# Kernel tuning notes

Measured on AMD Instinct MI355X. Metric: run time of the kernel, lower is better.

## Reference

```python
import jax, jax.numpy as jnp
import numpy as np

C = 256
EPS = 1e-5


def setup_inputs() -> dict:
    key = jax.random.key(0)
    ks = jax.random.split(key, 10)
    B, H, W = 4, 64, 64
    x1 = jax.random.normal(ks[0], (B, C, H, W), dtype=jnp.float32)
    x2 = jax.random.normal(ks[1], (B, C, H, W), dtype=jnp.float32)
    s = 1.0 / np.sqrt(C)
    qw = jax.random.normal(ks[2], (C, C), dtype=jnp.float32) * s
    qb = jax.random.normal(ks[3], (C,), dtype=jnp.float32) * 0.01
    kw = jax.random.normal(ks[4], (C, C), dtype=jnp.float32) * s
    kb = jax.random.normal(ks[5], (C,), dtype=jnp.float32) * 0.01
    vw = jax.random.normal(ks[6], (C, C), dtype=jnp.float32) * s
    vb = jax.random.normal(ks[7], (C,), dtype=jnp.float32) * 0.01
    ln_w = jnp.ones((C,), dtype=jnp.float32)
    ln_b = jnp.zeros((C,), dtype=jnp.float32)
    return {"x1": x1, "x2": x2, "qw": qw, "qb": qb, "kw": kw, "kb": kb,
            "vw": vw, "vb": vb, "ln_w": ln_w, "ln_b": ln_b}


def _conv1x1(x, w, b):
    # 1x1 conv == per-pixel matmul over channels. x: [B,C,H,W], w: [O,C]
    return jnp.einsum('oc,bchw->bohw', w, x) + b[None, :, None, None]


def reference(x1, x2, qw, qb, kw, kb, vw, vb, ln_w, ln_b):
    q = _conv1x1(x1, qw, qb)   # [B,C,H,W]
    k = _conv1x1(x2, kw, kb)   # [B,C,H,W]
    v = _conv1x1(x2, vw, vb)   # [B,C,H,W]
    # scores: [B,H,W,I,J]; softmax over LAST axis (j) only, as in the torch code
    scores = jnp.einsum('bchw,bcij->bhwij', q, k)
    attn = jax.nn.softmax(scores, axis=-1)
    fusion = jnp.einsum('bhwij,bcij->bchw', attn, v)  # [B,C,H,W]
    # LayerNorm2d: normalize over channel dim per spatial location
    mean = jnp.mean(fusion, axis=1, keepdims=True)
    var = jnp.var(fusion, axis=1, keepdims=True)
    normed = (fusion - mean) * jax.lax.rsqrt(var + EPS)
    return normed * ln_w[None, :, None, None] + ln_b[None, :, None, None]
```

## Files before the change

kernel.cpp:

```cpp
#include <hip/hip_runtime.h>


#define CDIM 256
#define NPOS 4096
#define BATCH 4
#define EPSV 1e-5f

typedef _Float16 f16;
typedef __attribute__((ext_vector_type(8))) _Float16 f16x8;
typedef __attribute__((ext_vector_type(4))) float f32x4;
typedef __attribute__((ext_vector_type(16))) float f32x16;

#define WST       264
#define QK_STRIDE 264
#define S_STRIDE  68
#define DQ_STRIDE 72
#define F_STRIDE  68

#define LBAR() asm volatile("s_waitcnt lgkmcnt(0)\n\ts_barrier" ::: "memory")


static __device__ __forceinline__ f16x8 cvt8(const float* __restrict__ p) {
    float4 w0 = *(const float4*)p;
    float4 w1 = *(const float4*)(p + 4);
    f16x8 r;
    r[0] = (f16)w0.x; r[1] = (f16)w0.y; r[2] = (f16)w0.z; r[3] = (f16)w0.w;
    r[4] = (f16)w1.x; r[5] = (f16)w1.y; r[6] = (f16)w1.z; r[7] = (f16)w1.w;
    return r;
}

__global__ __launch_bounds__(256, 4) void prep_kernel(
    const float* __restrict__ x1, const float* __restrict__ x2,
    const float* __restrict__ qw, const float* __restrict__ kw,
    const float* __restrict__ vw,
    f16* __restrict__ X1T, f16* __restrict__ X2T, f16* __restrict__ W16)
{
    const int id = blockIdx.x;
    const int t  = threadIdx.x;
    if (id < 2048) {
        __shared__ f16 T[64 * 72];
        const float* xs = (id & 1) ? x2 : x1;
        f16* dst        = (id & 1) ? X2T : X1T;
        const int t2 = id >> 1;
        const int b  = t2 >> 8;
        const int rm = t2 & 255;
        const int c0 = (rm >> 6) * 64;
        const int n0 = (rm & 63) * 64;
        const float* src = xs + ((size_t)b * CDIM + c0) * NPOS + n0;
        const int rr = t >> 6, col = t & 63;
        #pragma unroll
        for (int j = 0; j < 16; ++j) {
            int row = rr + j * 4;
            T[col * 72 + row] = (f16)src[(size_t)row * NPOS + col];
        }
        __syncthreads();
        const int n = t >> 3, lc = (t & 7) * 8;
        f16* d0 = dst + ((size_t)b * NPOS + n0) * CDIM + c0;
        #pragma unroll
        for (int j = 0; j < 2; ++j) {
            int nn = n + j * 32;
            *(f16x8*)(d0 + (size_t)nn * CDIM + lc) = *(const f16x8*)&T[nn * 72 + lc];
        }
    } else {
        const int wblk = id - 2048;
        const int pr = wblk >> 2, h = wblk & 3;
        const float* W = (pr == 0 ? qw : pr == 1 ? kw : vw) + (size_t)h * 64 * CDIM;
        f16* D = W16 + (size_t)pr * CDIM * CDIM + (size_t)h * 64 * CDIM;
        #pragma unroll
        for (int i = 0; i < 8; ++i) {
            int g = t + i * 256;
            int row = g >> 5, col = (g & 31) * 8;
            *(f16x8*)(D + (size_t)row * CDIM + col) = cvt8(W + (size_t)row * CDIM + col);
        }
    }
}

__global__ __launch_bounds__(256, 2) void gemm_kernel(
    const f16* __restrict__ X1T, const f16* __restrict__ X2T,
    const f16* __restrict__ W16,
    const float* __restrict__ qb, const float* __restrict__ kb,
    const float* __restrict__ vb,
    f16* __restrict__ Qg, f16* __restrict__ Kg, f16* __restrict__ Vg)
{
    __shared__ f16 Xs[64 * WST];
    __shared__ f16 Wh[64 * WST];
    __shared__ f16 Ds[64 * DQ_STRIDE];
    __shared__ float biasS[256];

    const int id = blockIdx.x;
    const int pr  = id >> 8;
    const int rem = id & 255;
    const int b   = rem >> 6;
    const int p0  = (rem & 63) << 6;
    const f16* XT = (pr == 0) ? X1T : X2T;
    const f16* Wp = W16 + (size_t)pr * CDIM * CDIM;
    const float* bias = pr == 0 ? qb : pr == 1 ? kb : vb;

    const int t = threadIdx.x, w = t >> 6, l = t & 63, lm = l & 31, lh = l >> 5;
    const int pt = w & 1, ot = w >> 1;

    biasS[t] = bias[t];
    #pragma unroll
    for (int it = 0; it < 8; ++it) {
        int p = w * 16 + it * 2 + lh;
        *(f16x8*)&Xs[p * WST + lm * 8] =
            *(const f16x8*)(XT + ((size_t)(b * NPOS + p0 + p)) * CDIM + lm * 8);
    }

    for (int q = 0; q < 4; ++q) {
        #pragma unroll
        for (int i = 0; i < 8; ++i) {
            int g = t + i * 256;
            int row = g >> 5, col = (g & 31) * 8;
            *(f16x8*)&Wh[row * WST + col] =
                *(const f16x8*)(Wp + (size_t)(q * 64 + row) * CDIM + col);
        }
        __syncthreads();

        f32x16 accA = {}, accB = {};
        #pragma unroll
        for (int ks = 0; ks < 16; ks += 2) {
            f16x8 x0 = *(const f16x8*)&Xs[(pt * 32 + lm) * WST + ks * 16 + lh * 8];
            f16x8 w0 = *(const f16x8*)&Wh[(ot * 32 + lm) * WST + ks * 16 + lh * 8];
            f16x8 x1v = *(const f16x8*)&Xs[(pt * 32 + lm) * WST + (ks + 1) * 16 + lh * 8];
            f16x8 w1 = *(const f16x8*)&Wh[(ot * 32 + lm) * WST + (ks + 1) * 16 + lh * 8];
            if (pr < 2) {
                accA = __builtin_amdgcn_mfma_f32_32x32x16_f16(x0, w0, accA, 0, 0, 0);
                accB = __builtin_amdgcn_mfma_f32_32x32x16_f16(x1v, w1, accB, 0, 0, 0);
            } else {
                accA = __builtin_amdgcn_mfma_f32_32x32x16_f16(w0, x0, accA, 0, 0, 0);
                accB = __builtin_amdgcn_mfma_f32_32x32x16_f16(w1, x1v, accB, 0, 0, 0);
            }
        }

        if (pr < 2) {
            int o_l = ot * 32 + lm;
            float bv = biasS[q * 64 + o_l];
            #pragma unroll
            for (int r = 0; r < 16; ++r) {
                int p_l = pt * 32 + (r & 3) + 8 * (r >> 2) + 4 * lh;
                Ds[p_l * DQ_STRIDE + o_l] = (f16)(accA[r] + accB[r] + bv);
            }
        } else {
            #pragma unroll
            for (int r = 0; r < 16; ++r) {
                int o_l = ot * 32 + (r & 3) + 8 * (r >> 2) + 4 * lh;
                Ds[o_l * DQ_STRIDE + pt * 32 + lm] =
                    (f16)(accA[r] + accB[r] + biasS[q * 64 + o_l]);
            }
        }
        __syncthreads();

        #pragma unroll
        for (int j = 0; j < 2; ++j) {
            int row = (t >> 3) + j * 32;
            int cc  = (t & 7) * 8;
            f16x8 vdat = *(const f16x8*)&Ds[row * DQ_STRIDE + cc];
            if (pr < 2) {
                f16* Out = (pr == 0) ? Qg : Kg;
                *(f16x8*)(Out + ((size_t)(b * NPOS + p0 + row)) * CDIM + q * 64 + cc) = vdat;
            } else {
                *(f16x8*)(Vg + ((size_t)(b * CDIM + q * 64 + row)) * NPOS + p0 + cc) = vdat;
            }
        }
        __syncthreads();
    }
}

__global__ __launch_bounds__(256, 2) void attn_kernel(
    const f16* __restrict__ Qg, const f16* __restrict__ Kg, const f16* __restrict__ Vg,
    float* __restrict__ Fp)
{
    __shared__ f16   Ks[64 * QK_STRIDE];
    __shared__ float Ss[64 * S_STRIDE];

    const int t    = threadIdx.x;
    const int L    = (int)((blockIdx.x & 7) * 64 + (blockIdx.x >> 3));
    const int grp  = L >> 6;
    const int b    = grp >> 1;
    const int half = grp & 1;
    const int qt   = L & 63;
    const int p0   = qt << 6;
    const int bq   = b * 64 + qt;
    const int w    = t >> 6;
    const int l    = t & 63;
    const int lm   = l & 31;
    const int lh   = l >> 5;
    const int spt  = w & 1;
    const int skt  = w >> 1;

    f16x8 qf[16];
    {
        const f16* qptr = Qg + (size_t)(b * NPOS + p0 + spt * 32 + lm) * CDIM + lh * 8;
        #pragma unroll
        for (int ks = 0; ks < 16; ++ks) qf[ks] = *(const f16x8*)(qptr + ks * 16);
    }

    const int kr = t >> 5, koff = (t & 31) * 8;
    f16x8 kreg[8];
    auto issue_k = [&](int ch) {
        const int i0 = ch * 64;
        #pragma unroll
        for (int r = 0; r < 8; ++r)
            kreg[r] = *(const f16x8*)(Kg + (size_t)(b * NPOS + i0 + r * 8 + kr) * CDIM + koff);
    };
    issue_k(half * 32);

    const f16* vb0 = Vg + (size_t)(b * CDIM + w * 64 + lm) * NPOS;
    const f16* vb1 = Vg + (size_t)(b * CDIM + w * 64 + 32 + lm) * NPOS;

    f16* Pal = (f16*)&Ss[0];

    f32x16 facc[4] = {};

    for (int it = 0; it < 32; ++it) {
        const int i0 = (half * 32 + it) * 64;

        #pragma unroll
        for (int r = 0; r < 8; ++r)
            *(f16x8*)&Ks[(r * 8 + kr) * QK_STRIDE + koff] = kreg[r];
        if (it < 31) issue_k(half * 32 + it + 1);
        LBAR();

        f16x8 vf0[4], vf1[4];
        #pragma unroll
        for (int ks = 0; ks < 4; ++ks) {
            vf0[ks] = *(const f16x8*)(vb0 + i0 + ks * 16 + lh * 8);
            vf1[ks] = *(const f16x8*)(vb1 + i0 + ks * 16 + lh * 8);
        }

        f32x16 sacc0 = {}, sacc1 = {};
        __builtin_amdgcn_s_setprio(1);
        #pragma unroll
        for (int ks = 0; ks < 16; ks += 2) {
            f16x8 b0 = *(const f16x8*)&Ks[(skt * 32 + lm) * QK_STRIDE + ks * 16 + lh * 8];
            f16x8 b1 = *(const f16x8*)&Ks[(skt * 32 + lm) * QK_STRIDE + (ks + 1) * 16 + lh * 8];
            sacc0 = __builtin_amdgcn_mfma_f32_32x32x16_f16(qf[ks], b0, sacc0, 0, 0, 0);
            sacc1 = __builtin_amdgcn_mfma_f32_32x32x16_f16(qf[ks + 1], b1, sacc1, 0, 0, 0);
        }
        __builtin_amdgcn_s_setprio(0);
        f32x16 sacc = sacc0 + sacc1;
        #pragma unroll
        for (int r = 0; r < 16; ++r) {
            int row = (r & 3) + 8 * (r >> 2) + 4 * lh;
            Ss[(spt * 32 + row) * S_STRIDE + skt * 32 + lm] = sacc[r];
        }
        LBAR();

        {
            const int r  = t >> 2;
            const int sg = (t & 3) * 16;
            const float* srow = &Ss[r * S_STRIDE + sg];
            float v[16];
            f32x4 a0 = *(const f32x4*)(srow);
            f32x4 a1 = *(const f32x4*)(srow + 4);
            f32x4 a2 = *(const f32x4*)(srow + 8);
            f32x4 a3 = *(const f32x4*)(srow + 12);
            v[0]=a0[0]; v[1]=a0[1]; v[2]=a0[2]; v[3]=a0[3];
            v[4]=a1[0]; v[5]=a1[1]; v[6]=a1[2]; v[7]=a1[3];
            v[8]=a2[0]; v[9]=a2[1]; v[10]=a2[2]; v[11]=a2[3];
            v[12]=a3[0]; v[13]=a3[1]; v[14]=a3[2]; v[15]=a3[3];
            float m = v[0];
            #pragma unroll
            for (int i = 1; i < 16; ++i) m = fmaxf(m, v[i]);
            m = fmaxf(m, __shfl_xor(m, 1));
            m = fmaxf(m, __shfl_xor(m, 2));
            float s = 0.f;
            #pragma unroll
            for (int i = 0; i < 16; ++i) { float e = __expf(v[i] - m); v[i] = e; s += e; }
            s += __shfl_xor(s, 1);
            s += __shfl_xor(s, 2);
            float inv = __builtin_amdgcn_rcpf(s);
            f16x8 h0, h1;
            #pragma unroll
            for (int i = 0; i < 8; ++i) { h0[i] = (f16)(v[i] * inv); h1[i] = (f16)(v[i + 8] * inv); }
            *(f16x8*)&Pal[r * 136 + sg]     = h0;
            *(f16x8*)&Pal[r * 136 + sg + 8] = h1;
        }
        LBAR();

        __builtin_amdgcn_s_setprio(1);
        #pragma unroll
        for (int ks = 0; ks < 4; ++ks) {
            f16x8 bp0 = *(const f16x8*)&Pal[lm * 136 + ks * 16 + lh * 8];
            f16x8 bp1 = *(const f16x8*)&Pal[(32 + lm) * 136 + ks * 16 + lh * 8];
            facc[0] = __builtin_amdgcn_mfma_f32_32x32x16_f16(vf0[ks], bp0, facc[0], 0, 0, 0);
            facc[1] = __builtin_amdgcn_mfma_f32_32x32x16_f16(vf0[ks], bp1, facc[1], 0, 0, 0);
            facc[2] = __builtin_amdgcn_mfma_f32_32x32x16_f16(vf1[ks], bp0, facc[2], 0, 0, 0);
            facc[3] = __builtin_amdgcn_mfma_f32_32x32x16_f16(vf1[ks], bp1, facc[3], 0, 0, 0);
        }
        __builtin_amdgcn_s_setprio(0);
    }

    float* dst = Fp + ((size_t)bq * 2 + half) * (CDIM * 64);
    #pragma unroll
    for (int ii = 0; ii < 2; ++ii)
        #pragma unroll
        for (int jj = 0; jj < 2; ++jj)
            #pragma unroll
            for (int r = 0; r < 16; ++r) {
                int c = w * 64 + ii * 32 + (r & 3) + 8 * (r >> 2) + 4 * lh;
                int p = jj * 32 + lm;
                dst[c * 64 + p] = facc[ii * 2 + jj][r];
            }
}

__global__ __launch_bounds__(256, 2) void merge_ln_kernel(
    const float* __restrict__ Fp, const float* __restrict__ ln_w,
    const float* __restrict__ ln_b, float* __restrict__ out)
{
    __shared__ float Fs[256 * F_STRIDE];
    __shared__ float redS[16 * 64], redQ[16 * 64];
    __shared__ float lnw_s[256], lnb_s[256];
    __shared__ float mu_s[64], rs_s[64];

    const int t  = threadIdx.x;
    const int bq = blockIdx.x;
    const int b  = bq >> 6;
    const int p0 = (bq & 63) << 6;

    lnw_s[t] = ln_w[t]; lnb_s[t] = ln_b[t];

    const int pb = (t & 15) * 4;
    const int cg = t >> 4;
    const float* base = Fp + (size_t)bq * 2 * (CDIM * 64);

    f32x4 s4 = {}, q4 = {};
    #pragma unroll 4
    for (int ci = 0; ci < 16; ++ci) {
        int c = cg * 16 + ci;
        size_t off = (size_t)c * 64 + pb;
        f32x4 v = *(const f32x4*)(base + off);
        v += *(const f32x4*)(base + (size_t)(CDIM * 64) + off);
        *(f32x4*)&Fs[c * F_STRIDE + pb] = v;
        s4 += v; q4 += v * v;
    }
    #pragma unroll
    for (int k2 = 0; k2 < 4; ++k2) {
        redS[cg * 64 + pb + k2] = s4[k2];
        redQ[cg * 64 + pb + k2] = q4[k2];
    }
    __syncthreads();
    if (t < 64) {
        float ss = 0.f, qq = 0.f;
        #pragma unroll
        for (int g2 = 0; g2 < 16; ++g2) { ss += redS[g2 * 64 + t]; qq += redQ[g2 * 64 + t]; }
        float mean = ss * (1.0f / 256.0f);
        float var  = qq * (1.0f / 256.0f) - mean * mean;
        mu_s[t] = mean;
        rs_s[t] = rsqrtf(var + EPSV);
    }
    __syncthreads();
    const int p   = t & 63;
    const int cg2 = t >> 6;
    const float mu = mu_s[p], rs = rs_s[p];
    float* dst = out + (size_t)b * CDIM * NPOS + p0 + p;
    #pragma unroll 4
    for (int ci = 0; ci < 64; ++ci) {
        int c = cg2 * 64 + ci;
        dst[(size_t)c * NPOS] = (Fs[c * F_STRIDE + p] - mu) * rs * lnw_s[c] + lnb_s[c];
    }
}

extern "C" void kernel_launch(void* const* d_in, const int* in_sizes, int n_in,
                              void* d_out, int out_size, void* d_ws, size_t ws_size,
                              hipStream_t stream)
{
    const float* x1  = (const float*)d_in[0];
    const float* x2  = (const float*)d_in[1];
    const float* qw  = (const float*)d_in[2];
    const float* qb  = (const float*)d_in[3];
    const float* kw  = (const float*)d_in[4];
    const float* kb  = (const float*)d_in[5];
    const float* vw  = (const float*)d_in[6];
    const float* vb  = (const float*)d_in[7];
    const float* lnw = (const float*)d_in[8];
    const float* lnb = (const float*)d_in[9];

    const size_t tsz = (size_t)BATCH * NPOS * CDIM;
    f16* Qg  = (f16*)d_ws;
    f16* Kg  = Qg + tsz;
    f16* Vg  = Kg + tsz;
    f16* X1T = Vg + tsz;
    f16* X2T = X1T + tsz;
    f16* W16 = X2T + tsz;
    float* Fp = (float*)X1T;

    prep_kernel<<<2060, 256, 0, stream>>>(x1, x2, qw, kw, vw, X1T, X2T, W16);
    gemm_kernel<<<768, 256, 0, stream>>>(X1T, X2T, W16, qb, kb, vb, Qg, Kg, Vg);
    attn_kernel<<<512, 256, 0, stream>>>(Qg, Kg, Vg, Fp);
    merge_ln_kernel<<<256, 256, 0, stream>>>(Fp, lnw, lnb, (float*)d_out);
}
```

Baseline: 217.8 us.

## Compute softmax in registers and stage V through LDS with prefetch

The score MFMA now computes the transposed tile (K as A operand), so each lane holds one query row's scores in registers. The row softmax is done in registers with a cross-half shuffle, and the two warps covering a row combine max and sum through a small LDS buffer. This replaces the fp32 score round-trip through shared memory. V chunks are now prefetched into registers one iteration ahead and staged in LDS, instead of each warp loading them directly from global memory inside the loop. LDS use per block grows (a 256x72 V buffer), which could reduce occupancy below the two-block launch bound.

```diff
diff --git a/kernel.cpp b/kernel.cpp
--- a/kernel.cpp
+++ b/kernel.cpp
@@ -7,13 +7,14 @@
 #define EPSV 1e-5f
 
 typedef _Float16 f16;
+typedef __attribute__((ext_vector_type(4))) _Float16 f16x4;
 typedef __attribute__((ext_vector_type(8))) _Float16 f16x8;
 typedef __attribute__((ext_vector_type(4))) float f32x4;
 typedef __attribute__((ext_vector_type(16))) float f32x16;
 
 #define WST       264
 #define QK_STRIDE 264
-#define S_STRIDE  68
+#define V_STRIDE  72
 #define DQ_STRIDE 72
 #define F_STRIDE  68
 
@@ -172,7 +173,9 @@
     float* __restrict__ Fp)
 {
     __shared__ f16   Ks[64 * QK_STRIDE];
-    __shared__ float Ss[64 * S_STRIDE];
+    __shared__ f16   Vs[256 * V_STRIDE];
+    __shared__ f16   Pl[64 * V_STRIDE];
+    __shared__ float RedM[2][64], RedS[2][64];
 
     const int t    = threadIdx.x;
     const int L    = (int)((blockIdx.x & 7) * 64 + (blockIdx.x >> 3));
@@ -204,90 +207,86 @@
         for (int r = 0; r < 8; ++r)
             kreg[r] = *(const f16x8*)(Kg + (size_t)(b * NPOS + i0 + r * 8 + kr) * CDIM + koff);
     };
+
+    const int vr = t >> 3;
+    const int vc = (t & 7) * 8;
+    f16x8 vreg[8];
+    auto issue_v = [&](int ch) {
+        const int i0 = ch * 64;
+        #pragma unroll
+        for (int i = 0; i < 8; ++i)
+            vreg[i] = *(const f16x8*)(Vg + (size_t)(b * CDIM + i * 32 + vr) * NPOS + i0 + vc);
+    };
+
     issue_k(half * 32);
-
-    const f16* vb0 = Vg + (size_t)(b * CDIM + w * 64 + lm) * NPOS;
-    const f16* vb1 = Vg + (size_t)(b * CDIM + w * 64 + 32 + lm) * NPOS;
-
-    f16* Pal = (f16*)&Ss[0];
+    issue_v(half * 32);
 
     f32x16 facc[4] = {};
 
     for (int it = 0; it < 32; ++it) {
-        const int i0 = (half * 32 + it) * 64;
+        const int ch = half * 32 + it;
 
         #pragma unroll
         for (int r = 0; r < 8; ++r)
             *(f16x8*)&Ks[(r * 8 + kr) * QK_STRIDE + koff] = kreg[r];
-        if (it < 31) issue_k(half * 32 + it + 1);
+        if (it < 31) issue_k(ch + 1);
         LBAR();
 
-        f16x8 vf0[4], vf1[4];
-        #pragma unroll
-        for (int ks = 0; ks < 4; ++ks) {
-            vf0[ks] = *(const f16x8*)(vb0 + i0 + ks * 16 + lh * 8);
-            vf1[ks] = *(const f16x8*)(vb1 + i0 + ks * 16 + lh * 8);
-        }
-
-        f32x16 sacc0 = {}, sacc1 = {};
+        #pragma unroll
+        for (int i = 0; i < 8; ++i)
+            *(f16x8*)&Vs[(i * 32 + vr) * V_STRIDE + vc] = vreg[i];
+        if (it < 31) issue_v(ch + 1);
+
+        f32x16 st = {};
         __builtin_amdgcn_s_setprio(1);
         #pragma unroll
-        for (int ks = 0; ks < 16; ks += 2) {
-            f16x8 b0 = *(const f16x8*)&Ks[(skt * 32 + lm) * QK_STRIDE + ks * 16 + lh * 8];
-            f16x8 b1 = *(const f16x8*)&Ks[(skt * 32 + lm) * QK_STRIDE + (ks + 1) * 16 + lh * 8];
-            sacc0 = __builtin_amdgcn_mfma_f32_32x32x16_f16(qf[ks], b0, sacc0, 0, 0, 0);
-            sacc1 = __builtin_amdgcn_mfma_f32_32x32x16_f16(qf[ks + 1], b1, sacc1, 0, 0, 0);
+        for (int ks = 0; ks < 16; ++ks) {
+            f16x8 kf = *(const f16x8*)&Ks[(skt * 32 + lm) * QK_STRIDE + ks * 16 + lh * 8];
+            st = __builtin_amdgcn_mfma_f32_32x32x16_f16(kf, qf[ks], st, 0, 0, 0);
         }
         __builtin_amdgcn_s_setprio(0);
-        f32x16 sacc = sacc0 + sacc1;
+
+        float mx = st[0];
+        #pragma unroll
+        for (int r = 1; r < 16; ++r) mx = fmaxf(mx, st[r]);
+        mx = fmaxf(mx, __shfl_xor(mx, 32));
+        float ss = 0.f;
         #pragma unroll
         for (int r = 0; r < 16; ++r) {
-            int row = (r & 3) + 8 * (r >> 2) + 4 * lh;
-            Ss[(spt * 32 + row) * S_STRIDE + skt * 32 + lm] = sacc[r];
-        }
+            float e = __expf(st[r] - mx);
+            st[r] = e;
+            ss += e;
+        }
+        ss += __shfl_xor(ss, 32);
+        if (lh == 0) { RedM[skt][spt * 32 + lm] = mx; RedS[skt][spt * 32 + lm] = ss; }
         LBAR();
 
-        {
-            const int r  = t >> 2;
-            const int sg = (t & 3) * 16;
-            const float* srow = &Ss[r * S_STRIDE + sg];
-            float v[16];
-            f32x4 a0 = *(const f32x4*)(srow);
-            f32x4 a1 = *(const f32x4*)(srow + 4);
-            f32x4 a2 = *(const f32x4*)(srow + 8);
-            f32x4 a3 = *(const f32x4*)(srow + 12);
-            v[0]=a0[0]; v[1]=a0[1]; v[2]=a0[2]; v[3]=a0[3];
-            v[4]=a1[0]; v[5]=a1[1]; v[6]=a1[2]; v[7]=a1[3];
-            v[8]=a2[0]; v[9]=a2[1]; v[10]=a2[2]; v[11]=a2[3];
-            v[12]=a3[0]; v[13]=a3[1]; v[14]=a3[2]; v[15]=a3[3];
-            float m = v[0];
+        float mo = RedM[skt ^ 1][spt * 32 + lm];
+        float so = RedS[skt ^ 1][spt * 32 + lm];
+        float M  = fmaxf(mx, mo);
+        float S  = ss * __expf(mx - M) + so * __expf(mo - M);
+        float scale = __expf(mx - M) * __builtin_amdgcn_rcpf(S);
+
+        #pragma unroll
+        for (int rq = 0; rq < 4; ++rq) {
+            f16x4 pk;
             #pragma unroll
-            for (int i = 1; i < 16; ++i) m = fmaxf(m, v[i]);
-            m = fmaxf(m, __shfl_xor(m, 1));
-            m = fmaxf(m, __shfl_xor(m, 2));
-            float s = 0.f;
-            #pragma unroll
-            for (int i = 0; i < 16; ++i) { float e = __expf(v[i] - m); v[i] = e; s += e; }
-            s += __shfl_xor(s, 1);
-            s += __shfl_xor(s, 2);
-            float inv = __builtin_amdgcn_rcpf(s);
-            f16x8 h0, h1;
-            #pragma unroll
-            for (int i = 0; i < 8; ++i) { h0[i] = (f16)(v[i] * inv); h1[i] = (f16)(v[i + 8] * inv); }
-            *(f16x8*)&Pal[r * 136 + sg]     = h0;
-            *(f16x8*)&Pal[r * 136 + sg + 8] = h1;
+            for (int q2 = 0; q2 < 4; ++q2) pk[q2] = (f16)(st[rq * 4 + q2] * scale);
+            *(f16x4*)&Pl[(spt * 32 + lm) * V_STRIDE + skt * 32 + rq * 8 + lh * 4] = pk;
         }
         LBAR();
 
         __builtin_amdgcn_s_setprio(1);
         #pragma unroll
-        for (int ks = 0; ks < 4; ++ks) {
-            f16x8 bp0 = *(const f16x8*)&Pal[lm * 136 + ks * 16 + lh * 8];
-            f16x8 bp1 = *(const f16x8*)&Pal[(32 + lm) * 136 + ks * 16 + lh * 8];
-            facc[0] = __builtin_amdgcn_mfma_f32_32x32x16_f16(vf0[ks], bp0, facc[0], 0, 0, 0);
-            facc[1] = __builtin_amdgcn_mfma_f32_32x32x16_f16(vf0[ks], bp1, facc[1], 0, 0, 0);
-            facc[2] = __builtin_amdgcn_mfma_f32_32x32x16_f16(vf1[ks], bp0, facc[2], 0, 0, 0);
-            facc[3] = __builtin_amdgcn_mfma_f32_32x32x16_f16(vf1[ks], bp1, facc[3], 0, 0, 0);
+        for (int kb = 0; kb < 4; ++kb) {
+            f16x8 pf0 = *(const f16x8*)&Pl[lm * V_STRIDE + kb * 16 + lh * 8];
+            f16x8 pf1 = *(const f16x8*)&Pl[(32 + lm) * V_STRIDE + kb * 16 + lh * 8];
+            f16x8 va0 = *(const f16x8*)&Vs[(w * 64 + lm) * V_STRIDE + kb * 16 + lh * 8];
+            f16x8 va1 = *(const f16x8*)&Vs[(w * 64 + 32 + lm) * V_STRIDE + kb * 16 + lh * 8];
+            facc[0] = __builtin_amdgcn_mfma_f32_32x32x16_f16(va0, pf0, facc[0], 0, 0, 0);
+            facc[1] = __builtin_amdgcn_mfma_f32_32x32x16_f16(va0, pf1, facc[1], 0, 0, 0);
+            facc[2] = __builtin_amdgcn_mfma_f32_32x32x16_f16(va1, pf0, facc[2], 0, 0, 0);
+            facc[3] = __builtin_amdgcn_mfma_f32_32x32x16_f16(va1, pf1, facc[3], 0, 0, 0);
         }
         __builtin_amdgcn_s_setprio(0);
     }
```

After: 217.1 us. No clear change (-0.4%).
